# Optimization experiments

Hardware: AMD Instinct MI355X
Metric: run time of the kernel (lower is better)

The kernel has to match this reference:

```python
import jax, jax.numpy as jnp
import numpy as np

S = 4          # num_subspaces
H = 1024       # hidden_dim
D = H // S     # subspace_dim = 256
B, N = 8, 1024
EPS = 1e-8


def setup_inputs() -> dict:
    key = jax.random.key(0)
    ks = jax.random.split(key, 6)
    sp = 1.0 / np.sqrt(H).astype(np.float32)
    sr = 1.0 / np.sqrt(D).astype(np.float32)
    return {
        "hx": jax.random.normal(ks[0], (B, N, H), jnp.float32),
        "ha": jax.random.normal(ks[1], (B, N, H), jnp.float32),
        "Wp": jax.random.normal(ks[2], (S, H, D), jnp.float32) * sp,  # stacked subspace_projs
        "bp": jax.random.normal(ks[3], (S, D), jnp.float32) * 0.01,
        "Wr": jax.random.normal(ks[4], (S, D, H), jnp.float32) * sr,  # stacked subspace_reconstructs
        "br": jax.random.normal(ks[5], (S, H), jnp.float32) * 0.01,
    }


def reference(hx, ha, Wp, bp, Wr, br):
    # Project into all subspaces at once: [S, B, N, D]
    x_sub = jnp.einsum('bnh,shd->sbnd', hx, Wp) + bp[:, None, None, :]
    a_sub = jnp.einsum('bnh,shd->sbnd', ha, Wp) + bp[:, None, None, :]

    # Cosine similarity = dot product of L2-normalized vectors (eps-clamped norms)
    xn = x_sub / jnp.maximum(jnp.linalg.norm(x_sub, axis=-1, keepdims=True), EPS)
    an = a_sub / jnp.maximum(jnp.linalg.norm(a_sub, axis=-1, keepdims=True), EPS)
    sim = jnp.einsum('sbid,sbjd->sbij', xn, an)       # [S, B, Nx, Na]

    # Softmax across the subspace axis (torch stacks sims then softmax(dim=0))
    w = jax.nn.softmax(sim, axis=0)                   # [S, B, Nx, Na]

    # Weighted aggregation per subspace, then reconstruct and sum over subspaces
    weighted = jnp.einsum('sbij,sbjd->sbid', w, a_sub)          # [S, B, Nx, D]
    out = jnp.einsum('sbid,sdh->bih', weighted, Wr) + br.sum(axis=0)  # [B, Nx, H]
    return out
```

## Files before the change

kernel.cpp:

```cpp
#include <hip/hip_runtime.h>
#include <hip/hip_bf16.h>

#define S_ 4
#define H_ 1024
#define D_ 256
#define B_ 8
#define N_ 1024
#define R_ (B_*N_)
#define EPS_ 1e-8f

typedef float f32x4 __attribute__((ext_vector_type(4)));
typedef short bf16x8 __attribute__((ext_vector_type(8)));
typedef unsigned short u16;

__device__ __forceinline__ u16 f2b(float f) {
    union { __bf16 h; u16 u; } cv; cv.h = (__bf16)f; return cv.u;
}

__device__ __forceinline__ void gload16(const void* g, void* l) {
    __builtin_amdgcn_global_load_lds((const __attribute__((address_space(1))) void*)g,
                                     (__attribute__((address_space(3))) void*)l, 16, 0, 0);
}

__device__ __forceinline__ void tc64(const float* __restrict__ src, int lds_,
                                     u16* __restrict__ dst, int ldd) {
    __shared__ float t[64][65];
    const int tid = threadIdx.x;
    const int rr = tid >> 4;
    const int cc = (tid & 15) * 4;
    #pragma unroll
    for (int p = 0; p < 4; ++p) {
        const int r = rr + p * 16;
        const float4 v = *(const float4*)(src + (size_t)r * lds_ + cc);
        t[r][cc] = v.x; t[r][cc + 1] = v.y; t[r][cc + 2] = v.z; t[r][cc + 3] = v.w;
    }
    __syncthreads();
    #pragma unroll
    for (int p = 0; p < 4; ++p) {
        const int c = rr + p * 16;
        union { u16 u[4]; uint2 v; } o;
        o.u[0] = f2b(t[cc + 0][c]); o.u[1] = f2b(t[cc + 1][c]);
        o.u[2] = f2b(t[cc + 2][c]); o.u[3] = f2b(t[cc + 3][c]);
        *(uint2*)(dst + (size_t)c * ldd + cc) = o.v;
    }
}

__global__ __launch_bounds__(256) void k_tc_wp(const float* __restrict__ Wp, u16* __restrict__ WpT) {
    const int s = blockIdx.z;
    const int r0 = blockIdx.x * 64;
    const int c0 = blockIdx.y * 64;
    tc64(Wp + (size_t)s * H_ * D_ + (size_t)r0 * D_ + c0, D_,
         WpT + (size_t)s * D_ * H_ + (size_t)c0 * H_ + r0, H_);
}

__global__ __launch_bounds__(256) void k_tc_wr(const float* __restrict__ Wr, u16* __restrict__ WrT) {
    const int r0 = blockIdx.y * 64;
    const int c0 = blockIdx.x * 64;
    tc64(Wr + (size_t)r0 * H_ + c0, H_,
         WrT + (size_t)c0 * H_ + r0, H_);
}

__global__ __launch_bounds__(256) void k_brsum(const float* __restrict__ br, float* __restrict__ bs) {
    const int h = blockIdx.x * 256 + threadIdx.x;
    if (h < H_) bs[h] = br[h] + br[H_ + h] + br[2 * H_ + h] + br[3 * H_ + h];
}

__global__ __launch_bounds__(256) void k_tc_araw(const u16* __restrict__ src, u16* __restrict__ dst) {
    const int sb = blockIdx.z, s = sb >> 3, b = sb & 7;
    const int j0 = blockIdx.x * 64, d0 = blockIdx.y * 64;
    __shared__ u16 tile[64][68];
    const int t = threadIdx.x;
    const int r = t >> 4, c4 = (t & 15) * 4;
    #pragma unroll
    for (int p = 0; p < 4; ++p) {
        const int row = p * 16 + r;
        *(uint2*)&tile[row][c4] =
            *(const uint2*)(src + (size_t)(b * N_ + j0 + row) * 1024 + s * 256 + d0 + c4);
    }
    __syncthreads();
    #pragma unroll
    for (int p = 0; p < 4; ++p) {
        const int orow = p * 16 + r;
        union { u16 u[4]; uint2 v; } o;
        o.u[0] = tile[c4 + 0][orow]; o.u[1] = tile[c4 + 1][orow];
        o.u[2] = tile[c4 + 2][orow]; o.u[3] = tile[c4 + 3][orow];
        *(uint2*)(dst + ((size_t)sb << 18) + (size_t)(d0 + orow) * 1024 + j0 + c4) = o.v;
    }
}

template<int WROWS, int WCOLS, int MFR, int NFR>
__device__ __forceinline__ void gemm_dbuf(
    const u16* __restrict__ Ag, const u16* __restrict__ Bg,
    int lda, int ldb, int K, u16* SA, u16* SB, f32x4 (&acc)[MFR][NFR])
{
    constexpr int NT = WROWS * WCOLS * 64;
    constexpr int TM = WROWS * MFR * 16;
    constexpr int TN = WCOLS * NFR * 16;
    constexpr int CA = TM * 8 / NT;
    constexpr int CB = TN * 8 / NT;
    constexpr int L  = CA + CB;
    const int tid = threadIdx.x, l = tid & 63, wv = tid >> 6;
    const int wm = wv / WCOLS, wn = wv % WCOLS;
    const int nsteps = K / 64;

    auto STAGE = [&](int buf, int k0) {
        #pragma unroll
        for (int i = 0; i < CA; ++i) {
            const int ci = i * NT + tid;
            const int row = ci >> 3, c = ci & 7, cs = c ^ (row & 7);
            gload16(Ag + (size_t)row * lda + k0 + cs * 8, SA + buf * TM * 64 + ci * 8);
        }
        #pragma unroll
        for (int i = 0; i < CB; ++i) {
            const int ci = i * NT + tid;
            const int row = ci >> 3, c = ci & 7, cs = c ^ (row & 7);
            gload16(Bg + (size_t)row * ldb + k0 + cs * 8, SB + buf * TN * 64 + ci * 8);
        }
    };

    STAGE(0, 0);
    for (int t = 0; t < nsteps; ++t) {
        const int cur = t & 1;
        if (t < nsteps - 1) {
            STAGE(cur ^ 1, (t + 1) * 64);
            if constexpr (L == 3)      asm volatile("s_waitcnt vmcnt(3)" ::: "memory");
            else if constexpr (L == 6) asm volatile("s_waitcnt vmcnt(6)" ::: "memory");
            else if constexpr (L == 8) asm volatile("s_waitcnt vmcnt(8)" ::: "memory");
            else                       asm volatile("s_waitcnt vmcnt(0)" ::: "memory");
        } else {
            asm volatile("s_waitcnt vmcnt(0)" ::: "memory");
        }
        __builtin_amdgcn_s_barrier();
        __builtin_amdgcn_sched_barrier(0);
        bf16x8 af[2][MFR], bq[2][NFR];
        #pragma unroll
        for (int kc = 0; kc < 2; ++kc) {
            #pragma unroll
            for (int m = 0; m < MFR; ++m) {
                const int r = wm * MFR * 16 + m * 16 + (l & 15);
                const int c = (kc * 4 + (l >> 4)) ^ (r & 7);
                af[kc][m] = *(const bf16x8*)(SA + cur * TM * 64 + r * 64 + c * 8);
            }
            #pragma unroll
            for (int n = 0; n < NFR; ++n) {
                const int r = wn * NFR * 16 + n * 16 + (l & 15);
                const int c = (kc * 4 + (l >> 4)) ^ (r & 7);
                bq[kc][n] = *(const bf16x8*)(SB + cur * TN * 64 + r * 64 + c * 8);
            }
        }
        asm volatile("s_waitcnt lgkmcnt(0)" ::: "memory");
        __builtin_amdgcn_s_barrier();
        __builtin_amdgcn_sched_barrier(0);
        #pragma unroll
        for (int kc = 0; kc < 2; ++kc)
            #pragma unroll
            for (int m = 0; m < MFR; ++m)
                #pragma unroll
                for (int n = 0; n < NFR; ++n)
                    acc[m][n] = __builtin_amdgcn_mfma_f32_16x16x32_bf16(af[kc][m], bq[kc][n], acc[m][n], 0, 0, 0);
    }
}

__global__ __launch_bounds__(512, 4) void k_proj_norm(
    const float* __restrict__ hx, const float* __restrict__ ha,
    const u16* __restrict__ WpT, const float* __restrict__ bp,
    u16* __restrict__ xnb, u16* __restrict__ araw, float* __restrict__ inv_na)
{
    __shared__ u16 SA[2][128][32];
    __shared__ u16 SB[2][256][32];
    __shared__ float normbuf[128][4];

    const int is_a = blockIdx.z;
    const int s  = blockIdx.y;
    const int rt = blockIdx.x * 128;
    const int tid = threadIdx.x;
    const int l = tid & 63, wv = tid >> 6;
    const int wm = wv >> 2, wn = wv & 3;
    const float* __restrict__ Ag = (is_a ? ha : hx) + (size_t)rt * 1024;
    const u16* __restrict__ Bg = WpT + (size_t)(s * 256) * 1024;

    const int arow = tid >> 2, aslot = tid & 3;
    const int acs  = (aslot - (arow >> 1)) & 3;
    const float* __restrict__ Ap = Ag + (size_t)arow * 1024 + acs * 8;

    f32x4 acc[4][4];
    #pragma unroll
    for (int m = 0; m < 4; ++m)
        #pragma unroll
        for (int n = 0; n < 4; ++n) acc[m][n] = (f32x4){0.f, 0.f, 0.f, 0.f};

    float4 a0[2], a1[2];
    auto ALOAD = [&](float4 (&r)[2], int k0) {
        r[0] = *(const float4*)(Ap + k0);
        r[1] = *(const float4*)(Ap + k0 + 4);
    };
    auto AWRITE = [&](const float4 (&r)[2], int buf) {
        union { u16 u[8]; uint4 v; } o;
        o.u[0] = f2b(r[0].x); o.u[1] = f2b(r[0].y); o.u[2] = f2b(r[0].z); o.u[3] = f2b(r[0].w);
        o.u[4] = f2b(r[1].x); o.u[5] = f2b(r[1].y); o.u[6] = f2b(r[1].z); o.u[7] = f2b(r[1].w);
        *(uint4*)&SA[buf][arow][aslot * 8] = o.v;
    };
    auto BSTAGE = [&](int buf, int k0) {
        #pragma unroll
        for (int i = 0; i < 2; ++i) {
            const int ci = i * 512 + tid;
            const int row = ci >> 2, c = ci & 3, cs = (c - (row >> 1)) & 3;
            gload16(Bg + (size_t)row * 1024 + k0 + cs * 8, &SB[buf][row][c * 8]);
        }
    };
    auto COMPUTE = [&](int cur) {
        bf16x8 af[4], bq[4];
        #pragma unroll
        for (int m = 0; m < 4; ++m) {
            const int r = wm * 64 + m * 16 + (l & 15);
            const int c = ((l >> 4) + (r >> 1)) & 3;
            af[m] = *(const bf16x8*)&SA[cur][r][c * 8];
        }
        #pragma unroll
        for (int n = 0; n < 4; ++n) {
            const int r = wn * 64 + n * 16 + (l & 15);
            const int c = ((l >> 4) + (r >> 1)) & 3;
            bq[n] = *(const bf16x8*)&SB[cur][r][c * 8];
        }
        asm volatile("s_waitcnt lgkmcnt(0)" ::: "memory");
        __builtin_amdgcn_sched_barrier(0);
        __builtin_amdgcn_s_barrier();
        __builtin_amdgcn_sched_barrier(0);
        #pragma unroll
        for (int m = 0; m < 4; ++m)
            #pragma unroll
            for (int n = 0; n < 4; ++n)
                acc[m][n] = __builtin_amdgcn_mfma_f32_16x16x32_bf16(af[m], bq[n], acc[m][n], 0, 0, 0);
    };
    auto BODY = [&](int t, float4 (&wset)[2], float4 (&lset)[2], int cur, bool doload) {
        asm volatile("s_waitcnt vmcnt(2)" ::: "memory");
        __builtin_amdgcn_sched_barrier(0);
        AWRITE(wset, cur ^ 1);
        if (doload) ALOAD(lset, (t + 2) * 32);
        BSTAGE(cur ^ 1, (t + 1) * 32);
        if (doload) asm volatile("s_waitcnt vmcnt(4)" ::: "memory");
        else        asm volatile("s_waitcnt vmcnt(2)" ::: "memory");
        asm volatile("s_waitcnt lgkmcnt(0)" ::: "memory");
        __builtin_amdgcn_sched_barrier(0);
        __builtin_amdgcn_s_barrier();
        __builtin_amdgcn_sched_barrier(0);
        COMPUTE(cur);
    };

    ALOAD(a0, 0);
    ALOAD(a1, 32);
    BSTAGE(0, 0);
    asm volatile("s_waitcnt vmcnt(4)" ::: "memory");
    __builtin_amdgcn_sched_barrier(0);
    AWRITE(a0, 0);

    for (int tt = 0; tt < 30; tt += 2) {
        BODY(tt,     a1, a0, 0, true);
        BODY(tt + 1, a0, a1, 1, true);
    }
    BODY(30, a1, a0, 0, false);
    asm volatile("s_waitcnt vmcnt(0)" ::: "memory");
    asm volatile("s_waitcnt lgkmcnt(0)" ::: "memory");
    __builtin_amdgcn_sched_barrier(0);
    __builtin_amdgcn_s_barrier();
    __builtin_amdgcn_sched_barrier(0);
    COMPUTE(1);

    float bv[4];
    #pragma unroll
    for (int n = 0; n < 4; ++n) bv[n] = bp[s * 256 + wn * 64 + n * 16 + (l & 15)];
    #pragma unroll
    for (int m = 0; m < 4; ++m)
        #pragma unroll
        for (int n = 0; n < 4; ++n)
            #pragma unroll
            for (int q = 0; q < 4; ++q) acc[m][n][q] += bv[n];

    float ss[4][4];
    #pragma unroll
    for (int m = 0; m < 4; ++m)
        #pragma unroll
        for (int q = 0; q < 4; ++q) {
            float v = 0.f;
            #pragma unroll
            for (int n = 0; n < 4; ++n) v += acc[m][n][q] * acc[m][n][q];
            ss[m][q] = v;
        }
    #pragma unroll
    for (int off = 1; off <= 8; off <<= 1)
        #pragma unroll
        for (int m = 0; m < 4; ++m)
            #pragma unroll
            for (int q = 0; q < 4; ++q) ss[m][q] += __shfl_xor(ss[m][q], off, 64);
    if ((l & 15) == 0) {
        #pragma unroll
        for (int m = 0; m < 4; ++m)
            #pragma unroll
            for (int q = 0; q < 4; ++q)
                normbuf[wm * 64 + m * 16 + (l >> 4) * 4 + q][wn] = ss[m][q];
    }
    __syncthreads();
    float sc[4][4];
    #pragma unroll
    for (int m = 0; m < 4; ++m)
        #pragma unroll
        for (int q = 0; q < 4; ++q) {
            const int rl = wm * 64 + m * 16 + (l >> 4) * 4 + q;
            const float tot = normbuf[rl][0] + normbuf[rl][1] + normbuf[rl][2] + normbuf[rl][3];
            sc[m][q] = 1.0f / fmaxf(sqrtf(tot), EPS_);
        }
    if (!is_a) {
        #pragma unroll
        for (int m = 0; m < 4; ++m)
            #pragma unroll
            for (int n = 0; n < 4; ++n)
                #pragma unroll
                for (int q = 0; q < 4; ++q) {
                    const int rl = wm * 64 + m * 16 + (l >> 4) * 4 + q;
                    xnb[(size_t)(rt + rl) * 1024 + s * 256 + wn * 64 + n * 16 + (l & 15)] =
                        f2b(acc[m][n][q] * sc[m][q]);
                }
    } else {
        #pragma unroll
        for (int m = 0; m < 4; ++m)
            #pragma unroll
            for (int n = 0; n < 4; ++n)
                #pragma unroll
                for (int q = 0; q < 4; ++q) {
                    const int rl = wm * 64 + m * 16 + (l >> 4) * 4 + q;
                    araw[(size_t)(rt + rl) * 1024 + s * 256 + wn * 64 + n * 16 + (l & 15)] =
                        f2b(acc[m][n][q]);
                }
        if (wn == 0 && (l & 15) == 0) {
            #pragma unroll
            for (int m = 0; m < 4; ++m)
                #pragma unroll
                for (int q = 0; q < 4; ++q) {
                    const int rl = wm * 64 + m * 16 + (l >> 4) * 4 + q;
                    inv_na[s * R_ + rt + rl] = sc[m][q];
                }
        }
    }
}

__global__ __launch_bounds__(512, 4) void k_sim_v3(
    const u16* __restrict__ xnb, const u16* __restrict__ araw,
    const float* __restrict__ inv_na, u16* __restrict__ whalf, const int half)
{
    __shared__ u16 SmA[2 * 64 * 64];
    __shared__ u16 SmB[2 * 128 * 64];
    const int b   = blockIdx.z;
    const int itl = blockIdx.y * 64;
    const int it  = half * 512 + itl;
    const int jt  = blockIdx.x * 128;
    const int tid = threadIdx.x, l = tid & 63, wv = tid >> 6;
    const int wi = wv >> 2, wj = wv & 3;
    const u16* __restrict__ Ag = xnb  + (size_t)(b * N_ + it) * 1024;
    const u16* __restrict__ Bg = araw + (size_t)(b * N_ + jt) * 1024;

    f32x4 acc[4][2][2];
    #pragma unroll
    for (int s = 0; s < 4; ++s)
        #pragma unroll
        for (int m = 0; m < 2; ++m)
            #pragma unroll
            for (int n = 0; n < 2; ++n) acc[s][m][n] = (f32x4){0.f, 0.f, 0.f, 0.f};

    auto STAGE = [&](int buf, int t) {
        const int k0 = t * 64;
        {
            const int ci = tid;
            const int row = ci >> 3, c = ci & 7, cs = c ^ (row & 7);
            gload16(Ag + (size_t)row * 1024 + k0 + cs * 8, SmA + buf * 4096 + ci * 8);
        }
        #pragma unroll
        for (int i = 0; i < 2; ++i) {
            const int ci = i * 512 + tid;
            const int row = ci >> 3, c = ci & 7, cs = c ^ (row & 7);
            gload16(Bg + (size_t)row * 1024 + k0 + cs * 8, SmB + buf * 8192 + ci * 8);
        }
    };

    STAGE(0, 0);
    #pragma unroll
    for (int s = 0; s < 4; ++s) {
        #pragma unroll
        for (int kk = 0; kk < 4; ++kk) {
            const int t = s * 4 + kk;
            const int cur = t & 1;
            if (t < 15) {
                STAGE(cur ^ 1, t + 1);
                asm volatile("s_waitcnt vmcnt(3)" ::: "memory");
            } else {
                asm volatile("s_waitcnt vmcnt(0)" ::: "memory");
            }
            __builtin_amdgcn_s_barrier();
            __builtin_amdgcn_sched_barrier(0);
            bf16x8 af[2][2], bq[2][2];
            #pragma unroll
            for (int kc = 0; kc < 2; ++kc) {
                #pragma unroll
                for (int m = 0; m < 2; ++m) {
                    const int r = wi * 32 + m * 16 + (l & 15);
                    const int c = (kc * 4 + (l >> 4)) ^ (r & 7);
                    af[kc][m] = *(const bf16x8*)(SmA + cur * 4096 + r * 64 + c * 8);
                }
                #pragma unroll
                for (int n = 0; n < 2; ++n) {
                    const int r = wj * 32 + n * 16 + (l & 15);
                    const int c = (kc * 4 + (l >> 4)) ^ (r & 7);
                    bq[kc][n] = *(const bf16x8*)(SmB + cur * 8192 + r * 64 + c * 8);
                }
            }
            asm volatile("s_waitcnt lgkmcnt(0)" ::: "memory");
            __builtin_amdgcn_s_barrier();
            __builtin_amdgcn_sched_barrier(0);
            #pragma unroll
            for (int kc = 0; kc < 2; ++kc)
                #pragma unroll
                for (int m = 0; m < 2; ++m)
                    #pragma unroll
                    for (int n = 0; n < 2; ++n)
                        acc[s][m][n] = __builtin_amdgcn_mfma_f32_16x16x32_bf16(
                            af[kc][m], bq[kc][n], acc[s][m][n], 0, 0, 0);
        }
    }

    #pragma unroll
    for (int n = 0; n < 2; ++n) {
        const int jg = jt + wj * 32 + n * 16 + (l & 15);
        float inv[4];
        #pragma unroll
        for (int s = 0; s < 4; ++s) inv[s] = inv_na[s * R_ + b * N_ + jg];
        #pragma unroll
        for (int m = 0; m < 2; ++m)
            #pragma unroll
            for (int q = 0; q < 4; ++q) {
                const int il = itl + wi * 32 + m * 16 + (l >> 4) * 4 + q;
                float e[4]; float sum = 0.f;
                #pragma unroll
                for (int s = 0; s < 4; ++s) { e[s] = __expf(acc[s][m][n][q] * inv[s]); sum += e[s]; }
                const float rs = 1.0f / sum;
                #pragma unroll
                for (int s = 0; s < 4; ++s)
                    whalf[((size_t)(s * B_ + b) << 19) + (size_t)il * 1024 + jg] = f2b(e[s] * rs);
            }
    }
}

__global__ __launch_bounds__(256, 2) void k_gemm_weighted(
    const u16* __restrict__ whalf, const u16* __restrict__ arawT,
    u16* __restrict__ weighted, const int half)
{
    __shared__ u16 SA[2 * 64 * 64];
    __shared__ u16 SB[2 * 128 * 64];
    const int sb = blockIdx.z, s = sb >> 3, b = sb & 7;
    const int mt = blockIdx.y * 64, nt = blockIdx.x * 128;
    f32x4 acc[2][4];
    #pragma unroll
    for (int m = 0; m < 2; ++m)
        #pragma unroll
        for (int n = 0; n < 4; ++n) acc[m][n] = (f32x4){0.f, 0.f, 0.f, 0.f};
    gemm_dbuf<2, 2, 2, 4>(whalf + ((size_t)sb << 19) + (size_t)mt * 1024,
                          arawT + ((size_t)sb << 18) + (size_t)nt * 1024,
                          1024, 1024, 1024, SA, SB, acc);
    const int l = threadIdx.x & 63, wv = threadIdx.x >> 6;
    const int wm = wv >> 1, wn = wv & 1;
    #pragma unroll
    for (int m = 0; m < 2; ++m)
        #pragma unroll
        for (int n = 0; n < 4; ++n)
            #pragma unroll
            for (int q = 0; q < 4; ++q) {
                const int i = half * 512 + mt + wm * 32 + m * 16 + (l >> 4) * 4 + q;
                const int d = nt + wn * 64 + n * 16 + (l & 15);
                weighted[(size_t)(b * N_ + i) * 1024 + s * 256 + d] = f2b(acc[m][n][q]);
            }
}

__global__ __launch_bounds__(256, 2) void k_gemm_recon(
    const u16* __restrict__ weighted, const u16* __restrict__ WrT,
    const float* __restrict__ brsum, float* __restrict__ out)
{
    __shared__ u16 SA[2 * 128 * 64];
    __shared__ u16 SB[2 * 128 * 64];
    const int mt = blockIdx.y * 128, nt = blockIdx.x * 128;
    f32x4 acc[4][4];
    #pragma unroll
    for (int m = 0; m < 4; ++m)
        #pragma unroll
        for (int n = 0; n < 4; ++n) acc[m][n] = (f32x4){0.f, 0.f, 0.f, 0.f};
    gemm_dbuf<2, 2, 4, 4>(weighted + (size_t)mt * 1024, WrT + (size_t)nt * 1024,
                          1024, 1024, 1024, SA, SB, acc);
    const int l = threadIdx.x & 63, wv = threadIdx.x >> 6;
    const int wm = wv >> 1, wn = wv & 1;
    #pragma unroll
    for (int m = 0; m < 4; ++m)
        #pragma unroll
        for (int n = 0; n < 4; ++n)
            #pragma unroll
            for (int q = 0; q < 4; ++q) {
                const int row = mt + wm * 64 + m * 16 + (l >> 4) * 4 + q;
                const int col = nt + wn * 64 + n * 16 + (l & 15);
                out[(size_t)row * 1024 + col] = acc[m][n][q] + brsum[col];
            }
}

extern "C" void kernel_launch(void* const* d_in, const int* in_sizes, int n_in,
                              void* d_out, int out_size, void* d_ws, size_t ws_size,
                              hipStream_t stream) {
    const float* hx = (const float*)d_in[0];
    const float* ha = (const float*)d_in[1];
    const float* Wp = (const float*)d_in[2];
    const float* bp = (const float*)d_in[3];
    const float* Wr = (const float*)d_in[4];
    const float* br = (const float*)d_in[5];
    float* out = (float*)d_out;

    char* W = (char*)d_ws;
    u16* WpT      = (u16*)(W + (32ull << 20));
    u16* WrT      = (u16*)(W + (34ull << 20));
    float* brsum  = (float*)(W + (36ull << 20));
    float* inv_na = (float*)(W + (36ull << 20) + (256ull << 10));
    u16* xnb      = (u16*)(W + (37ull << 20));
    u16* araw     = (u16*)(W + (53ull << 20));
    u16* arawT    = (u16*)(W + (69ull << 20));
    u16* whalf    = (u16*)(W + (85ull << 20));
    u16* weighted = (u16*)(W);

    k_tc_wp<<<dim3(16, 4, 4), dim3(256), 0, stream>>>(Wp, WpT);
    k_tc_wr<<<dim3(16, 16), dim3(256), 0, stream>>>(Wr, WrT);
    k_brsum<<<dim3(4), dim3(256), 0, stream>>>(br, brsum);

    k_proj_norm<<<dim3(64, 4, 2), dim3(512), 0, stream>>>(hx, ha, WpT, bp, xnb, araw, inv_na);

    k_tc_araw<<<dim3(16, 4, 32), dim3(256), 0, stream>>>(araw, arawT);

    for (int half = 0; half < 2; ++half) {
        k_sim_v3<<<dim3(8, 8, 8), dim3(512), 0, stream>>>(xnb, araw, inv_na, whalf, half);
        k_gemm_weighted<<<dim3(2, 8, 32), dim3(256), 0, stream>>>(whalf, arawT, weighted, half);
    }

    k_gemm_recon<<<dim3(8, 64), dim3(256), 0, stream>>>(weighted, WrT, brsum, out);
}
```

Before: 178.2 us.

## Fuse araw transpose into projection epilogue and merge weight-prep kernels

The separate kernel that transposed the bf16 projected `a` tensor is removed. `k_proj_norm` now stages its output tile in shared memory and writes the transposed `arawT` layout directly, so the extra 16 MB read/write pass and one launch go away. The three small weight and bias preparation kernels are merged into a single launch that dispatches on block index. In exchange, shared memory per block roughly doubles to fit the transpose tile, which may lower occupancy of the projection GEMM, and the epilogue gains two extra barriers.

```diff
diff --git a/kernel.cpp b/kernel.cpp
--- a/kernel.cpp
+++ b/kernel.cpp
@@ -45,46 +45,26 @@
     }
 }
 
-__global__ __launch_bounds__(256) void k_tc_wp(const float* __restrict__ Wp, u16* __restrict__ WpT) {
-    const int s = blockIdx.z;
-    const int r0 = blockIdx.x * 64;
-    const int c0 = blockIdx.y * 64;
-    tc64(Wp + (size_t)s * H_ * D_ + (size_t)r0 * D_ + c0, D_,
-         WpT + (size_t)s * D_ * H_ + (size_t)c0 * H_ + r0, H_);
-}
-
-__global__ __launch_bounds__(256) void k_tc_wr(const float* __restrict__ Wr, u16* __restrict__ WrT) {
-    const int r0 = blockIdx.y * 64;
-    const int c0 = blockIdx.x * 64;
-    tc64(Wr + (size_t)r0 * H_ + c0, H_,
-         WrT + (size_t)c0 * H_ + r0, H_);
-}
-
-__global__ __launch_bounds__(256) void k_brsum(const float* __restrict__ br, float* __restrict__ bs) {
-    const int h = blockIdx.x * 256 + threadIdx.x;
-    if (h < H_) bs[h] = br[h] + br[H_ + h] + br[2 * H_ + h] + br[3 * H_ + h];
-}
-
-__global__ __launch_bounds__(256) void k_tc_araw(const u16* __restrict__ src, u16* __restrict__ dst) {
-    const int sb = blockIdx.z, s = sb >> 3, b = sb & 7;
-    const int j0 = blockIdx.x * 64, d0 = blockIdx.y * 64;
-    __shared__ u16 tile[64][68];
-    const int t = threadIdx.x;
-    const int r = t >> 4, c4 = (t & 15) * 4;
-    #pragma unroll
-    for (int p = 0; p < 4; ++p) {
-        const int row = p * 16 + r;
-        *(uint2*)&tile[row][c4] =
-            *(const uint2*)(src + (size_t)(b * N_ + j0 + row) * 1024 + s * 256 + d0 + c4);
-    }
-    __syncthreads();
-    #pragma unroll
-    for (int p = 0; p < 4; ++p) {
-        const int orow = p * 16 + r;
-        union { u16 u[4]; uint2 v; } o;
-        o.u[0] = tile[c4 + 0][orow]; o.u[1] = tile[c4 + 1][orow];
-        o.u[2] = tile[c4 + 2][orow]; o.u[3] = tile[c4 + 3][orow];
-        *(uint2*)(dst + ((size_t)sb << 18) + (size_t)(d0 + orow) * 1024 + j0 + c4) = o.v;
+__global__ __launch_bounds__(256) void k_prep(
+    const float* __restrict__ Wp, const float* __restrict__ Wr, const float* __restrict__ br,
+    u16* __restrict__ WpT, u16* __restrict__ WrT, float* __restrict__ brsum)
+{
+    const int bid = blockIdx.x;
+    if (bid < 256) {
+        const int s = bid >> 6;
+        const int r0 = (bid & 15) * 64;
+        const int c0 = ((bid >> 4) & 3) * 64;
+        tc64(Wp + (size_t)s * H_ * D_ + (size_t)r0 * D_ + c0, D_,
+             WpT + (size_t)s * D_ * H_ + (size_t)c0 * H_ + r0, H_);
+    } else if (bid < 512) {
+        const int b2 = bid - 256;
+        const int c0 = (b2 & 15) * 64;
+        const int r0 = (b2 >> 4) * 64;
+        tc64(Wr + (size_t)r0 * H_ + c0, H_,
+             WrT + (size_t)c0 * H_ + r0, H_);
+    } else {
+        const int h = (bid - 512) * 256 + threadIdx.x;
+        if (h < H_) brsum[h] = br[h] + br[H_ + h] + br[2 * H_ + h] + br[3 * H_ + h];
     }
 }
 
@@ -164,11 +144,14 @@
 __global__ __launch_bounds__(512, 4) void k_proj_norm(
     const float* __restrict__ hx, const float* __restrict__ ha,
     const u16* __restrict__ WpT, const float* __restrict__ bp,
-    u16* __restrict__ xnb, u16* __restrict__ araw, float* __restrict__ inv_na)
+    u16* __restrict__ xnb, u16* __restrict__ araw, float* __restrict__ inv_na,
+    u16* __restrict__ arawT)
 {
-    __shared__ u16 SA[2][128][32];
-    __shared__ u16 SB[2][256][32];
-    __shared__ float normbuf[128][4];
+    __shared__ __align__(16) char smem[67840];
+    u16 (*SA)[128][32] = (u16(*)[128][32])smem;
+    u16 (*SB)[256][32] = (u16(*)[256][32])(smem + 16384);
+    u16 (*T)[257]      = (u16(*)[257])smem;
+    float (*normbuf)[4] = (float(*)[4])(smem + 65792);
 
     const int is_a = blockIdx.z;
     const int s  = blockIdx.y;
@@ -337,8 +320,30 @@
                 #pragma unroll
                 for (int q = 0; q < 4; ++q) {
                     const int rl = wm * 64 + m * 16 + (l >> 4) * 4 + q;
-                    inv_na[s * R_ + rt + rl] = sc[m][q];
+                    inv_na[s * R_ + rt + rl] = sc[q][0] * 0.f + sc[m][q];
                 }
+        }
+        __syncthreads();
+        #pragma unroll
+        for (int m = 0; m < 4; ++m)
+            #pragma unroll
+            for (int n = 0; n < 4; ++n)
+                #pragma unroll
+                for (int q = 0; q < 4; ++q) {
+                    const int rl = wm * 64 + m * 16 + (l >> 4) * 4 + q;
+                    T[rl][wn * 64 + n * 16 + (l & 15)] = f2b(acc[m][n][q]);
+                }
+        __syncthreads();
+        const size_t abase = ((size_t)(s * B_ + (rt >> 10)) << 18);
+        const int j0 = rt & 1023;
+        #pragma unroll
+        for (int p = 0; p < 8; ++p) {
+            const int idx = p * 512 + tid;
+            const int d = idx >> 4, jg = (idx & 15) * 8;
+            union { u16 u[8]; uint4 v; } o;
+            #pragma unroll
+            for (int jj = 0; jj < 8; ++jj) o.u[jj] = T[jg + jj][d];
+            *(uint4*)(arawT + abase + (size_t)d * 1024 + j0 + jg) = o.v;
         }
     }
 }
@@ -528,13 +533,9 @@
     u16* whalf    = (u16*)(W + (85ull << 20));
     u16* weighted = (u16*)(W);
 
-    k_tc_wp<<<dim3(16, 4, 4), dim3(256), 0, stream>>>(Wp, WpT);
-    k_tc_wr<<<dim3(16, 16), dim3(256), 0, stream>>>(Wr, WrT);
-    k_brsum<<<dim3(4), dim3(256), 0, stream>>>(br, brsum);
-
-    k_proj_norm<<<dim3(64, 4, 2), dim3(512), 0, stream>>>(hx, ha, WpT, bp, xnb, araw, inv_na);
-
-    k_tc_araw<<<dim3(16, 4, 32), dim3(256), 0, stream>>>(araw, arawT);
+    k_prep<<<dim3(516), dim3(256), 0, stream>>>(Wp, Wr, br, WpT, WrT, brsum);
+
+    k_proj_norm<<<dim3(64, 4, 2), dim3(512), 0, stream>>>(hx, ha, WpT, bp, xnb, araw, inv_na, arawT);
 
     for (int half = 0; half < 2; ++half) {
         k_sim_v3<<<dim3(8, 8, 8), dim3(512), 0, stream>>>(xnb, araw, inv_na, whalf, half);
```

New measurement: 193.1 us. 1.08x slower.
